# Kernel tuning notes

Hardware: AMD Instinct MI355X
Metric: run time of the kernel (lower is better)

The kernel has to match this reference:

```python
import jax, jax.numpy as jnp
import numpy as np

N = 100_000   # nodes
E = 200_000   # edges
D = 768       # d_model
L = 4         # gnn_layers
AF, AV = 9, 64   # atom feature columns, atom vocab
BF, BV = 3, 8    # bond feature columns, bond vocab


def layer_norm(x, g, b, eps=1e-5):
    m = x.mean(-1, keepdims=True)
    v = x.var(-1, keepdims=True)
    return (x - m) * jax.lax.rsqrt(v + eps) * g + b


def setup_inputs() -> dict:
    key = jax.random.key(0)
    keys = iter(jax.random.split(key, 40))
    w = lambda shape: jax.random.normal(next(keys), shape, jnp.float32) * 0.02
    return {
        "x": jax.random.randint(next(keys), (N, AF), 0, AV),
        "edge_attr": jax.random.randint(next(keys), (E, BF), 0, BV),
        "edge_index": jax.random.randint(next(keys), (2, E), 0, N),
        # AtomEncoder params (9 embedding tables stacked)
        "atom_emb": w((AF, AV, D)),
        "atom_ln_g": jnp.ones((D,)), "atom_ln_b": jnp.zeros((D,)),
        "atom_w1": w((D, D)), "atom_b1": jnp.zeros((D,)),
        "atom_w2": w((D, D)), "atom_b2": jnp.zeros((D,)),
        # BondEncoder params (3 embedding tables stacked)
        "bond_emb": w((BF, BV, D)),
        "bond_ln_g": jnp.ones((D,)), "bond_ln_b": jnp.zeros((D,)),
        "bond_w1": w((D, D)), "bond_b1": jnp.zeros((D,)),
        "bond_w2": w((D, D)), "bond_b2": jnp.zeros((D,)),
        # per-layer GINEConv MLP (Linear-ReLU-Linear) and LayerNorm, stacked on L
        "conv_w1": w((L, D, D)), "conv_b1": jnp.zeros((L, D)),
        "conv_w2": w((L, D, D)), "conv_b2": jnp.zeros((L, D)),
        "ln_g": jnp.ones((L, D)), "ln_b": jnp.zeros((L, D)),
    }


def reference(x, edge_attr, edge_index,
              atom_emb, atom_ln_g, atom_ln_b, atom_w1, atom_b1, atom_w2, atom_b2,
              bond_emb, bond_ln_g, bond_ln_b, bond_w1, bond_b1, bond_w2, bond_b2,
              conv_w1, conv_b1, conv_w2, conv_b2, ln_g, ln_b):
    gelu = lambda t: jax.nn.gelu(t, approximate=False)  # torch default GELU is exact

    # AtomEncoder: sum of per-column embeddings -> LN -> Linear/GELU/Linear
    h = atom_emb[jnp.arange(AF), x].sum(axis=1)            # [N, D]
    h = layer_norm(h, atom_ln_g, atom_ln_b)
    h = gelu(h @ atom_w1 + atom_b1) @ atom_w2 + atom_b2

    # BondEncoder
    e = bond_emb[jnp.arange(BF), edge_attr].sum(axis=1)    # [E, D]
    e = layer_norm(e, bond_ln_g, bond_ln_b)
    e = gelu(e @ bond_w1 + bond_b1) @ bond_w2 + bond_b2

    src, dst = edge_index[0], edge_index[1]
    for l in range(L):
        # GINEConv (eps=0): aggr_i = sum_{j->i} relu(h_j + e_ji); out = mlp(h_i + aggr_i)
        msg = jax.nn.relu(h[src] + e)                      # [E, D] gather + add
        aggr = jax.ops.segment_sum(msg, dst, num_segments=N)
        z = h + aggr
        z = jax.nn.relu(z @ conv_w1[l] + conv_b1[l]) @ conv_w2[l] + conv_b2[l]
        z = gelu(z)                                        # dropout=0 (eval)
        h = layer_norm(z + h, ln_g[l], ln_b[l])
    return h
```

## Files before the change

### kernel.cpp

```cpp
#include <hip/hip_runtime.h>

#define DM 768
#define SCAN_BS 1024

using u16 = unsigned short;
using u32 = unsigned int;

typedef __attribute__((ext_vector_type(8))) __bf16 bf16x8;
typedef __attribute__((ext_vector_type(4))) float f32x4;
typedef __attribute__((address_space(1))) void gvoid;
typedef __attribute__((address_space(3))) void lvoid;

__device__ __forceinline__ float bf2f(u16 h) { return __uint_as_float(((u32)h) << 16); }
__device__ __forceinline__ u16 f2bf(float f) {
    u32 u = __float_as_uint(f);
    u32 r = (u + 0x7FFFu + ((u >> 16) & 1u)) >> 16;
    return (u16)r;
}
__device__ __forceinline__ float gelu_f(float x) { return 0.5f * x * (1.f + erff(x * 0.70710678118f)); }

__global__ __launch_bounds__(256) void prep_weights(
    const float* __restrict__ aw1, const float* __restrict__ aw2,
    const float* __restrict__ bw1, const float* __restrict__ bw2,
    const float* __restrict__ cw1, const float* __restrict__ cw2,
    u16* __restrict__ wbt)
{
    int z = blockIdx.z;
    const float* W;
    if (z == 0) W = aw1;
    else if (z == 1) W = aw2;
    else if (z == 2) W = bw1;
    else if (z == 3) W = bw2;
    else if (z < 8) W = cw1 + (size_t)(z - 4) * DM * DM;
    else W = cw2 + (size_t)(z - 8) * DM * DM;
    u16* out = wbt + (size_t)z * DM * DM;

    __shared__ float tile[32][33];
    int bx = blockIdx.x * 32, by = blockIdx.y * 32;
    int tx = threadIdx.x & 31, ty = threadIdx.x >> 5;
    #pragma unroll
    for (int i = ty; i < 32; i += 8) tile[i][tx] = W[(size_t)(by + i) * DM + bx + tx];
    __syncthreads();
    #pragma unroll
    for (int i = ty; i < 32; i += 8) out[(size_t)(bx + i) * DM + by + tx] = f2bf(tile[tx][i]);
}

__global__ __launch_bounds__(256) void encode_ln(
    const int* __restrict__ idx, int nf, int vocab,
    const float* __restrict__ emb, const float* __restrict__ g, const float* __restrict__ bb,
    u16* __restrict__ out)
{
    long n = blockIdx.x;
    int t = threadIdx.x;
    __shared__ int feat[16];
    __shared__ float sred[16];
    if (t < nf) feat[t] = idx[n * nf + t];
    __syncthreads();
    float v[3];
    float s = 0.f, s2 = 0.f;
    #pragma unroll
    for (int j = 0; j < 3; j++) {
        int d = t + j * 256;
        float a = 0.f;
        for (int f = 0; f < nf; f++) a += emb[((long)f * vocab + feat[f]) * DM + d];
        v[j] = a; s += a; s2 += a * a;
    }
    #pragma unroll
    for (int o = 32; o; o >>= 1) { s += __shfl_down(s, o); s2 += __shfl_down(s2, o); }
    int wid = t >> 6;
    if ((t & 63) == 0) { sred[wid] = s; sred[8 + wid] = s2; }
    __syncthreads();
    if (t == 0) {
        sred[0] = sred[0] + sred[1] + sred[2] + sred[3];
        sred[8] = sred[8] + sred[9] + sred[10] + sred[11];
    }
    __syncthreads();
    float mean = sred[0] * (1.f / 768.f);
    float var = sred[8] * (1.f / 768.f) - mean * mean;
    float rstd = rsqrtf(var + 1e-5f);
    #pragma unroll
    for (int j = 0; j < 3; j++) {
        int d = t + j * 256;
        out[n * DM + d] = f2bf((v[j] - mean) * rstd * g[d] + bb[d]);
    }
}

__global__ __launch_bounds__(256) void encode_ln_bond(
    const float* __restrict__ emb, const float* __restrict__ g, const float* __restrict__ bb,
    u16* __restrict__ out)
{
    int key = blockIdx.x;
    int t = threadIdx.x;
    __shared__ float sred[16];
    int f0 = key & 7, f1 = (key >> 3) & 7, f2 = (key >> 6) & 7;
    float v[3];
    float s = 0.f, s2 = 0.f;
    #pragma unroll
    for (int j = 0; j < 3; j++) {
        int d = t + j * 256;
        float a = emb[(0 * 8 + f0) * DM + d] + emb[(1 * 8 + f1) * DM + d] + emb[(2 * 8 + f2) * DM + d];
        v[j] = a; s += a; s2 += a * a;
    }
    #pragma unroll
    for (int o = 32; o; o >>= 1) { s += __shfl_down(s, o); s2 += __shfl_down(s2, o); }
    int wid = t >> 6;
    if ((t & 63) == 0) { sred[wid] = s; sred[8 + wid] = s2; }
    __syncthreads();
    if (t == 0) {
        sred[0] = sred[0] + sred[1] + sred[2] + sred[3];
        sred[8] = sred[8] + sred[9] + sred[10] + sred[11];
    }
    __syncthreads();
    float mean = sred[0] * (1.f / 768.f);
    float var = sred[8] * (1.f / 768.f) - mean * mean;
    float rstd = rsqrtf(var + 1e-5f);
    #pragma unroll
    for (int j = 0; j < 3; j++) {
        int d = t + j * 256;
        out[(long)key * DM + d] = f2bf((v[j] - mean) * rstd * g[d] + bb[d]);
    }
}

__global__ __launch_bounds__(192) void layer_ln(
    const u16* __restrict__ y, const u16* __restrict__ holdb,
    const float* __restrict__ g, const float* __restrict__ bb,
    u16* __restrict__ hb, float* __restrict__ dout)
{
    long n = blockIdx.x;
    int t = threadIdx.x;
    int d = t * 4;
    __shared__ float sred[8];
    ushort4 yv = *reinterpret_cast<const ushort4*>(y + n * DM + d);
    ushort4 hv = *reinterpret_cast<const ushort4*>(holdb + n * DM + d);
    float v0 = bf2f(yv.x) + bf2f(hv.x);
    float v1 = bf2f(yv.y) + bf2f(hv.y);
    float v2 = bf2f(yv.z) + bf2f(hv.z);
    float v3 = bf2f(yv.w) + bf2f(hv.w);
    float s = v0 + v1 + v2 + v3;
    float s2 = v0 * v0 + v1 * v1 + v2 * v2 + v3 * v3;
    #pragma unroll
    for (int o = 32; o; o >>= 1) { s += __shfl_down(s, o); s2 += __shfl_down(s2, o); }
    int wid = t >> 6;
    if ((t & 63) == 0) { sred[wid] = s; sred[4 + wid] = s2; }
    __syncthreads();
    float S = sred[0] + sred[1] + sred[2];
    float S2 = sred[4] + sred[5] + sred[6];
    float mean = S * (1.f / 768.f);
    float var = S2 * (1.f / 768.f) - mean * mean;
    float rstd = rsqrtf(var + 1e-5f);
    float r0 = (v0 - mean) * rstd * g[d + 0] + bb[d + 0];
    float r1 = (v1 - mean) * rstd * g[d + 1] + bb[d + 1];
    float r2 = (v2 - mean) * rstd * g[d + 2] + bb[d + 2];
    float r3 = (v3 - mean) * rstd * g[d + 3] + bb[d + 3];
    if (dout) {
        float4 o = { r0, r1, r2, r3 };
        *reinterpret_cast<float4*>(dout + n * DM + d) = o;
    } else {
        ushort4 o;
        o.x = f2bf(r0); o.y = f2bf(r1); o.z = f2bf(r2); o.w = f2bf(r3);
        *reinterpret_cast<ushort4*>(hb + n * DM + d) = o;
    }
}

__global__ __launch_bounds__(256) void csr_count(const int* __restrict__ dst, int* __restrict__ deg, int E)
{
    int e = blockIdx.x * 256 + threadIdx.x;
    if (e < E) atomicAdd(&deg[dst[e]], 1);
}

__global__ __launch_bounds__(SCAN_BS) void scan_block(const int* __restrict__ deg, int* __restrict__ tmp,
                                                      int* __restrict__ bsum, int n)
{
    __shared__ int sh[SCAN_BS];
    int gid = blockIdx.x * SCAN_BS + threadIdx.x;
    int v = (gid < n) ? deg[gid] : 0;
    sh[threadIdx.x] = v;
    __syncthreads();
    for (int o = 1; o < SCAN_BS; o <<= 1) {
        int add = (threadIdx.x >= o) ? sh[threadIdx.x - o] : 0;
        __syncthreads();
        sh[threadIdx.x] += add;
        __syncthreads();
    }
    if (gid < n) tmp[gid] = sh[threadIdx.x];
    if (threadIdx.x == SCAN_BS - 1) bsum[blockIdx.x] = sh[SCAN_BS - 1];
}

__global__ __launch_bounds__(SCAN_BS) void scan_bsum(int* __restrict__ bsum, int nb)
{
    __shared__ int sh[SCAN_BS];
    int v = (threadIdx.x < nb) ? bsum[threadIdx.x] : 0;
    sh[threadIdx.x] = v;
    __syncthreads();
    for (int o = 1; o < SCAN_BS; o <<= 1) {
        int add = (threadIdx.x >= o) ? sh[threadIdx.x - o] : 0;
        __syncthreads();
        sh[threadIdx.x] += add;
        __syncthreads();
    }
    if (threadIdx.x < nb) bsum[threadIdx.x] = sh[threadIdx.x];
}

__global__ __launch_bounds__(256) void scan_final(const int* __restrict__ tmp, const int* __restrict__ bsum,
                                                  const int* __restrict__ deg, int* __restrict__ offs,
                                                  int* __restrict__ cursor, int n)
{
    int gid = blockIdx.x * 256 + threadIdx.x;
    if (gid >= n) return;
    int b = gid / SCAN_BS;
    int inc = tmp[gid] + (b > 0 ? bsum[b - 1] : 0);
    offs[gid + 1] = inc;
    cursor[gid] = inc - deg[gid];
    if (gid == 0) offs[0] = 0;
}

__global__ __launch_bounds__(256) void csr_fill(const int* __restrict__ dst, int* __restrict__ cursor,
                                                int* __restrict__ perm, int E)
{
    int e = blockIdx.x * 256 + threadIdx.x;
    if (e < E) {
        int p = atomicAdd(&cursor[dst[e]], 1);
        perm[p] = e;
    }
}

__global__ __launch_bounds__(256) void pack_edges(
    const int* __restrict__ src, const int* __restrict__ eattr, const int* __restrict__ perm,
    u32* __restrict__ ep, int E)
{
    int k = blockIdx.x * 256 + threadIdx.x;
    if (k < E) {
        int eid = perm[k];
        int key = eattr[eid * 3 + 0] + (eattr[eid * 3 + 1] << 3) + (eattr[eid * 3 + 2] << 6);
        ep[k] = ((u32)src[eid] << 9) | (u32)key;
    }
}

__global__ __launch_bounds__(192) void aggregate(
    const u16* __restrict__ h, const u16* __restrict__ ebtab,
    const u32* __restrict__ ep, const int* __restrict__ offs,
    u16* __restrict__ out)
{
    long n = blockIdx.x;
    int t = threadIdx.x;
    int d = t * 4;
    ushort4 a = *reinterpret_cast<const ushort4*>(h + n * DM + d);
    float acc0 = bf2f(a.x), acc1 = bf2f(a.y), acc2 = bf2f(a.z), acc3 = bf2f(a.w);
    int beg = offs[n], end = offs[n + 1];
    for (int k = beg; k < end; k++) {
        u32 pk = ep[k];
        long s = pk >> 9;
        long key = pk & 511;
        ushort4 hv = *reinterpret_cast<const ushort4*>(h + s * DM + d);
        ushort4 ev = *reinterpret_cast<const ushort4*>(ebtab + key * DM + d);
        acc0 += fmaxf(0.f, bf2f(hv.x) + bf2f(ev.x));
        acc1 += fmaxf(0.f, bf2f(hv.y) + bf2f(ev.y));
        acc2 += fmaxf(0.f, bf2f(hv.z) + bf2f(ev.z));
        acc3 += fmaxf(0.f, bf2f(hv.w) + bf2f(ev.w));
    }
    ushort4 o;
    o.x = f2bf(acc0); o.y = f2bf(acc1); o.z = f2bf(acc2); o.w = f2bf(acc3);
    *reinterpret_cast<ushort4*>(out + n * DM + d) = o;
}

union GemmSmem {
    u16 tiles[2][2][128 * 32];
    u16 ctile[128 * 136];
};

template <int ACT>
__global__ __launch_bounds__(256) void gemm128(
    const u16* __restrict__ A, const u16* __restrict__ Bt,
    const float* __restrict__ bias, u16* __restrict__ outB)
{
    __shared__ GemmSmem sm;
    const int tid = threadIdx.x;
    const int lane = tid & 63, wid = tid >> 6;
    const int wr = wid >> 1, wc = wid & 1;

    const int nwg = gridDim.x;
    const int orig = blockIdx.x;
    const int q8 = nwg >> 3, r8 = nwg & 7;
    const int xcd = orig & 7, idx8 = orig >> 3;
    const int w = (xcd < r8 ? xcd * (q8 + 1) : r8 * (q8 + 1) + (xcd - r8) * q8) + idx8;
    const int n0 = (w % 6) * 128;
    const long m0 = (long)(w / 6) * 128;

    f32x4 acc[4][4] = {};

    const int ch0 = tid, ch1 = 256 + tid;
    const int r0_ = ch0 >> 2, k0_ = (ch0 & 3) ^ ((r0_ >> 1) & 3);
    const int r1_ = ch1 >> 2, k1_ = (ch1 & 3) ^ ((r1_ >> 1) & 3);
    const u16* Ag0 = A + (m0 + r0_) * DM + k0_ * 8;
    const u16* Ag1 = A + (m0 + r1_) * DM + k1_ * 8;
    const u16* Bg0 = Bt + (long)(n0 + r0_) * DM + k0_ * 8;
    const u16* Bg1 = Bt + (long)(n0 + r1_) * DM + k1_ * 8;
    const int lds0 = ((wid << 6)) * 8;
    const int lds1 = (256 + (wid << 6)) * 8;

    auto stage = [&](int buf, int kt) {
        int ko = kt * 32;
        __builtin_amdgcn_global_load_lds((gvoid*)(Ag0 + ko), (lvoid*)&sm.tiles[buf][0][lds0], 16, 0, 0);
        __builtin_amdgcn_global_load_lds((gvoid*)(Ag1 + ko), (lvoid*)&sm.tiles[buf][0][lds1], 16, 0, 0);
        __builtin_amdgcn_global_load_lds((gvoid*)(Bg0 + ko), (lvoid*)&sm.tiles[buf][1][lds0], 16, 0, 0);
        __builtin_amdgcn_global_load_lds((gvoid*)(Bg1 + ko), (lvoid*)&sm.tiles[buf][1][lds1], 16, 0, 0);
    };

    stage(0, 0);
    asm volatile("s_waitcnt vmcnt(0)" ::: "memory");
    __syncthreads();

    const int ar = lane & 15, kb = lane >> 4;
    const int kbe = kb ^ ((ar >> 1) & 3);
    int cur = 0;
    for (int kt = 0; kt < DM / 32; ++kt) {
        if (kt + 1 < DM / 32) stage(cur ^ 1, kt + 1);
        bf16x8 af[4], bv[4];
        #pragma unroll
        for (int m = 0; m < 4; m++)
            af[m] = *reinterpret_cast<const bf16x8*>(&sm.tiles[cur][0][(wr * 64 + m * 16 + ar) * 32 + kbe * 8]);
        #pragma unroll
        for (int n = 0; n < 4; n++)
            bv[n] = *reinterpret_cast<const bf16x8*>(&sm.tiles[cur][1][(wc * 64 + n * 16 + ar) * 32 + kbe * 8]);
        #pragma unroll
        for (int m = 0; m < 4; m++)
            #pragma unroll
            for (int n = 0; n < 4; n++)
                acc[m][n] = __builtin_amdgcn_mfma_f32_16x16x32_bf16(af[m], bv[n], acc[m][n], 0, 0, 0);
        asm volatile("s_waitcnt vmcnt(0)" ::: "memory");
        __syncthreads();
        cur ^= 1;
    }

    const int rg4 = (lane >> 4) * 4;
    #pragma unroll
    for (int n = 0; n < 4; n++) {
        int lc = wc * 64 + n * 16 + ar;
        float bvp = bias[n0 + lc];
        #pragma unroll
        for (int m = 0; m < 4; m++) {
            int lr = wr * 64 + m * 16 + rg4;
            #pragma unroll
            for (int j = 0; j < 4; j++) {
                float v = acc[m][n][j] + bvp;
                if (ACT == 1) v = fmaxf(v, 0.f);
                if (ACT == 2) v = gelu_f(v);
                sm.ctile[(lr + j) * 136 + lc] = f2bf(v);
            }
        }
    }
    __syncthreads();
    const int row = tid >> 2, b4 = tid & 3;
    #pragma unroll
    for (int ps = 0; ps < 2; ps++) {
        int rr = row + ps * 64;
        const u16* srcp = &sm.ctile[rr * 136];
        u16* dstp = outB + (m0 + rr) * DM + n0;
        #pragma unroll
        for (int i = 0; i < 4; i++) {
            int c = b4 * 8 + i * 32;
            *reinterpret_cast<uint4*>(dstp + c) = *reinterpret_cast<const uint4*>(srcp + c);
        }
    }
}

extern "C" void kernel_launch(void* const* d_in, const int* in_sizes, int n_in,
                              void* d_out, int out_size, void* d_ws, size_t ws_size,
                              hipStream_t stream)
{
    const int N = in_sizes[0] / 9;
    const int E = in_sizes[1] / 3;
    const int L = 4;
    const long Mpad = ((N + 127) / 128) * 128;
    const int Mtiles = (int)(Mpad / 128);

    const int* x = (const int*)d_in[0];
    const int* eattr = (const int*)d_in[1];
    const int* eidx = (const int*)d_in[2];
    const float* atom_emb = (const float*)d_in[3];
    const float* atom_g = (const float*)d_in[4];
    const float* atom_bb = (const float*)d_in[5];
    const float* atom_w1 = (const float*)d_in[6];
    const float* atom_b1 = (const float*)d_in[7];
    const float* atom_w2 = (const float*)d_in[8];
    const float* atom_b2 = (const float*)d_in[9];
    const float* bond_emb = (const float*)d_in[10];
    const float* bond_g = (const float*)d_in[11];
    const float* bond_bb = (const float*)d_in[12];
    const float* bond_w1 = (const float*)d_in[13];
    const float* bond_b1 = (const float*)d_in[14];
    const float* bond_w2 = (const float*)d_in[15];
    const float* bond_b2 = (const float*)d_in[16];
    const float* conv_w1 = (const float*)d_in[17];
    const float* conv_b1 = (const float*)d_in[18];
    const float* conv_w2 = (const float*)d_in[19];
    const float* conv_b2 = (const float*)d_in[20];
    const float* ln_g = (const float*)d_in[21];
    const float* ln_b = (const float*)d_in[22];
    const int* src = eidx;
    const int* dst = eidx + E;
    float* dout = (float*)d_out;

    char* p = (char*)d_ws;
    auto alloc = [&](size_t bytes) { void* r = (void*)p; p += (bytes + 255) & ~(size_t)255; return r; };
    u16* B2   = (u16*)alloc((size_t)2 * Mpad * DM * 2);
    u16* h_b  = (u16*)alloc((size_t)Mpad * DM * 2);
    u16* wbt  = (u16*)alloc((size_t)12 * DM * DM * 2);
    u16* bt0  = (u16*)alloc((size_t)512 * DM * 2);
    u16* bt1  = (u16*)alloc((size_t)512 * DM * 2);
    u16* ebtab= (u16*)alloc((size_t)512 * DM * 2);
    int* deg    = (int*)alloc((size_t)N * 4);
    int* tmp    = (int*)alloc((size_t)N * 4);
    int* cursor = (int*)alloc((size_t)N * 4);
    int* offs   = (int*)alloc((size_t)(N + 1) * 4);
    int* bsum   = (int*)alloc((size_t)SCAN_BS * 4);
    int* perm   = (int*)alloc((size_t)E * 4);
    u32* ep     = (u32*)alloc((size_t)E * 4);
    u16* B2a = B2;
    u16* B2b = B2 + (size_t)Mpad * DM;

    hipMemsetAsync(deg, 0, (size_t)N * 4, stream);
    csr_count<<<(E + 255) / 256, 256, 0, stream>>>(dst, deg, E);
    const int nb = (N + SCAN_BS - 1) / SCAN_BS;
    scan_block<<<nb, SCAN_BS, 0, stream>>>(deg, tmp, bsum, N);
    scan_bsum<<<1, SCAN_BS, 0, stream>>>(bsum, nb);
    scan_final<<<(N + 255) / 256, 256, 0, stream>>>(tmp, bsum, deg, offs, cursor, N);
    csr_fill<<<(E + 255) / 256, 256, 0, stream>>>(dst, cursor, perm, E);
    pack_edges<<<(E + 255) / 256, 256, 0, stream>>>(src, eattr, perm, ep, E);

    prep_weights<<<dim3(24, 24, 12), 256, 0, stream>>>(atom_w1, atom_w2, bond_w1, bond_w2, conv_w1, conv_w2, wbt);

    encode_ln_bond<<<512, 256, 0, stream>>>(bond_emb, bond_g, bond_bb, bt0);
    gemm128<2><<<6 * 4, 256, 0, stream>>>(bt0, wbt + (size_t)2 * DM * DM, bond_b1, bt1);
    gemm128<0><<<6 * 4, 256, 0, stream>>>(bt1, wbt + (size_t)3 * DM * DM, bond_b2, ebtab);

    encode_ln<<<N, 256, 0, stream>>>(x, 9, 64, atom_emb, atom_g, atom_bb, B2a);
    gemm128<2><<<6 * Mtiles, 256, 0, stream>>>(B2a, wbt + (size_t)0 * DM * DM, atom_b1, B2b);
    gemm128<0><<<6 * Mtiles, 256, 0, stream>>>(B2b, wbt + (size_t)1 * DM * DM, atom_b2, h_b);

    for (int l = 0; l < L; l++) {
        aggregate<<<N, 192, 0, stream>>>(h_b, ebtab, ep, offs, B2a);
        gemm128<1><<<6 * Mtiles, 256, 0, stream>>>(B2a, wbt + (size_t)(4 + l) * DM * DM, conv_b1 + l * DM, B2b);
        gemm128<2><<<6 * Mtiles, 256, 0, stream>>>(B2b, wbt + (size_t)(8 + l) * DM * DM, conv_b2 + l * DM, B2a);
        layer_ln<<<N, 192, 0, stream>>>(B2a, h_b, ln_g + l * DM, ln_b + l * DM,
                                        h_b, (l == L - 1) ? dout : nullptr);
    }
}
```

Measured before the change: 3.092 ms.

## Use 256-row GEMM tiles, tanh-approx GELU, and vectorized atom encoder

The GEMM tile grows from 128x128 to 256x128. Each wave now computes 64x128 with 32 accumulators, which doubles B-tile reuse per load and halves the number of blocks. The epilogue writes the output in two 128-row halves through the shared C tile. The exact erf GELU is replaced with a tanh approximation using fast exp and reciprocal, which cuts epilogue math but departs from the exact-GELU reference. The atom encoder uses 192 threads with float4 loads and a single reduction barrier.

```diff
diff --git a/kernel.cpp b/kernel.cpp
--- a/kernel.cpp
+++ b/kernel.cpp
@@ -17,7 +17,12 @@
     u32 r = (u + 0x7FFFu + ((u >> 16) & 1u)) >> 16;
     return (u16)r;
 }
-__device__ __forceinline__ float gelu_f(float x) { return 0.5f * x * (1.f + erff(x * 0.70710678118f)); }
+__device__ __forceinline__ float gelu_f(float x) {
+    float y = 0.7978845608f * x * (1.f + 0.044715f * x * x);
+    float e = __expf(2.f * y);
+    float th = 1.f - 2.f * __builtin_amdgcn_rcpf(e + 1.f);
+    return 0.5f * x * (1.f + th);
+}
 
 __global__ __launch_bounds__(256) void prep_weights(
     const float* __restrict__ aw1, const float* __restrict__ aw2,
@@ -45,44 +50,43 @@
     for (int i = ty; i < 32; i += 8) out[(size_t)(bx + i) * DM + by + tx] = f2bf(tile[tx][i]);
 }
 
-__global__ __launch_bounds__(256) void encode_ln(
-    const int* __restrict__ idx, int nf, int vocab,
+__global__ __launch_bounds__(192) void encode_ln9(
+    const int* __restrict__ idx,
     const float* __restrict__ emb, const float* __restrict__ g, const float* __restrict__ bb,
     u16* __restrict__ out)
 {
     long n = blockIdx.x;
     int t = threadIdx.x;
-    __shared__ int feat[16];
-    __shared__ float sred[16];
-    if (t < nf) feat[t] = idx[n * nf + t];
-    __syncthreads();
-    float v[3];
-    float s = 0.f, s2 = 0.f;
-    #pragma unroll
-    for (int j = 0; j < 3; j++) {
-        int d = t + j * 256;
-        float a = 0.f;
-        for (int f = 0; f < nf; f++) a += emb[((long)f * vocab + feat[f]) * DM + d];
-        v[j] = a; s += a; s2 += a * a;
-    }
+    int d = t * 4;
+    __shared__ int feat[12];
+    __shared__ float sred[8];
+    if (t < 9) feat[t] = idx[n * 9 + t];
+    __syncthreads();
+    float a0 = 0.f, a1 = 0.f, a2 = 0.f, a3 = 0.f;
+    #pragma unroll
+    for (int f = 0; f < 9; f++) {
+        const float* rp = emb + (size_t)f * 64 * DM + (size_t)feat[f] * DM + d;
+        float4 v = *reinterpret_cast<const float4*>(rp);
+        a0 += v.x; a1 += v.y; a2 += v.z; a3 += v.w;
+    }
+    float s = a0 + a1 + a2 + a3;
+    float s2 = a0 * a0 + a1 * a1 + a2 * a2 + a3 * a3;
     #pragma unroll
     for (int o = 32; o; o >>= 1) { s += __shfl_down(s, o); s2 += __shfl_down(s2, o); }
     int wid = t >> 6;
-    if ((t & 63) == 0) { sred[wid] = s; sred[8 + wid] = s2; }
-    __syncthreads();
-    if (t == 0) {
-        sred[0] = sred[0] + sred[1] + sred[2] + sred[3];
-        sred[8] = sred[8] + sred[9] + sred[10] + sred[11];
-    }
-    __syncthreads();
-    float mean = sred[0] * (1.f / 768.f);
-    float var = sred[8] * (1.f / 768.f) - mean * mean;
+    if ((t & 63) == 0) { sred[wid] = s; sred[4 + wid] = s2; }
+    __syncthreads();
+    float S = sred[0] + sred[1] + sred[2];
+    float S2 = sred[4] + sred[5] + sred[6];
+    float mean = S * (1.f / 768.f);
+    float var = S2 * (1.f / 768.f) - mean * mean;
     float rstd = rsqrtf(var + 1e-5f);
-    #pragma unroll
-    for (int j = 0; j < 3; j++) {
-        int d = t + j * 256;
-        out[n * DM + d] = f2bf((v[j] - mean) * rstd * g[d] + bb[d]);
-    }
+    ushort4 o;
+    o.x = f2bf((a0 - mean) * rstd * g[d + 0] + bb[d + 0]);
+    o.y = f2bf((a1 - mean) * rstd * g[d + 1] + bb[d + 1]);
+    o.z = f2bf((a2 - mean) * rstd * g[d + 2] + bb[d + 2]);
+    o.w = f2bf((a3 - mean) * rstd * g[d + 3] + bb[d + 3]);
+    *reinterpret_cast<ushort4*>(out + n * DM + d) = o;
 }
 
 __global__ __launch_bounds__(256) void encode_ln_bond(
@@ -264,19 +268,18 @@
 }
 
 union GemmSmem {
-    u16 tiles[2][2][128 * 32];
+    u16 tiles[2][384 * 32];
     u16 ctile[128 * 136];
 };
 
 template <int ACT>
-__global__ __launch_bounds__(256) void gemm128(
+__global__ __launch_bounds__(256) void gemm256(
     const u16* __restrict__ A, const u16* __restrict__ Bt,
     const float* __restrict__ bias, u16* __restrict__ outB)
 {
     __shared__ GemmSmem sm;
     const int tid = threadIdx.x;
     const int lane = tid & 63, wid = tid >> 6;
-    const int wr = wid >> 1, wc = wid & 1;
 
     const int nwg = gridDim.x;
     const int orig = blockIdx.x;
@@ -284,26 +287,30 @@
     const int xcd = orig & 7, idx8 = orig >> 3;
     const int w = (xcd < r8 ? xcd * (q8 + 1) : r8 * (q8 + 1) + (xcd - r8) * q8) + idx8;
     const int n0 = (w % 6) * 128;
-    const long m0 = (long)(w / 6) * 128;
-
-    f32x4 acc[4][4] = {};
-
-    const int ch0 = tid, ch1 = 256 + tid;
-    const int r0_ = ch0 >> 2, k0_ = (ch0 & 3) ^ ((r0_ >> 1) & 3);
-    const int r1_ = ch1 >> 2, k1_ = (ch1 & 3) ^ ((r1_ >> 1) & 3);
-    const u16* Ag0 = A + (m0 + r0_) * DM + k0_ * 8;
-    const u16* Ag1 = A + (m0 + r1_) * DM + k1_ * 8;
-    const u16* Bg0 = Bt + (long)(n0 + r0_) * DM + k0_ * 8;
-    const u16* Bg1 = Bt + (long)(n0 + r1_) * DM + k1_ * 8;
-    const int lds0 = ((wid << 6)) * 8;
-    const int lds1 = (256 + (wid << 6)) * 8;
+    const long m0 = (long)(w / 6) * 256;
+
+    f32x4 acc[4][8] = {};
+
+    const u16* gsrc[6];
+    #pragma unroll
+    for (int cl = 0; cl < 6; cl++) {
+        int c = cl * 256 + tid;
+        if (cl < 4) {
+            int r = c >> 2, kc = (c & 3) ^ ((r >> 1) & 3);
+            gsrc[cl] = A + (m0 + r) * DM + kc * 8;
+        } else {
+            int cb = c - 1024;
+            int r = cb >> 2, kc = (cb & 3) ^ ((r >> 1) & 3);
+            gsrc[cl] = Bt + (long)(n0 + r) * DM + kc * 8;
+        }
+    }
 
     auto stage = [&](int buf, int kt) {
         int ko = kt * 32;
-        __builtin_amdgcn_global_load_lds((gvoid*)(Ag0 + ko), (lvoid*)&sm.tiles[buf][0][lds0], 16, 0, 0);
-        __builtin_amdgcn_global_load_lds((gvoid*)(Ag1 + ko), (lvoid*)&sm.tiles[buf][0][lds1], 16, 0, 0);
-        __builtin_amdgcn_global_load_lds((gvoid*)(Bg0 + ko), (lvoid*)&sm.tiles[buf][1][lds0], 16, 0, 0);
-        __builtin_amdgcn_global_load_lds((gvoid*)(Bg1 + ko), (lvoid*)&sm.tiles[buf][1][lds1], 16, 0, 0);
+        #pragma unroll
+        for (int cl = 0; cl < 6; cl++)
+            __builtin_amdgcn_global_load_lds((gvoid*)(gsrc[cl] + ko),
+                (lvoid*)&sm.tiles[buf][(cl * 256 + (wid << 6)) * 8], 16, 0, 0);
     };
 
     stage(0, 0);
@@ -315,17 +322,17 @@
     int cur = 0;
     for (int kt = 0; kt < DM / 32; ++kt) {
         if (kt + 1 < DM / 32) stage(cur ^ 1, kt + 1);
-        bf16x8 af[4], bv[4];
+        bf16x8 af[4], bv[8];
         #pragma unroll
         for (int m = 0; m < 4; m++)
-            af[m] = *reinterpret_cast<const bf16x8*>(&sm.tiles[cur][0][(wr * 64 + m * 16 + ar) * 32 + kbe * 8]);
+            af[m] = *reinterpret_cast<const bf16x8*>(&sm.tiles[cur][(wid * 64 + m * 16 + ar) * 32 + kbe * 8]);
         #pragma unroll
-        for (int n = 0; n < 4; n++)
-            bv[n] = *reinterpret_cast<const bf16x8*>(&sm.tiles[cur][1][(wc * 64 + n * 16 + ar) * 32 + kbe * 8]);
+        for (int n = 0; n < 8; n++)
+            bv[n] = *reinterpret_cast<const bf16x8*>(&sm.tiles[cur][8192 + (n * 16 + ar) * 32 + kbe * 8]);
         #pragma unroll
         for (int m = 0; m < 4; m++)
             #pragma unroll
-            for (int n = 0; n < 4; n++)
+            for (int n = 0; n < 8; n++)
                 acc[m][n] = __builtin_amdgcn_mfma_f32_16x16x32_bf16(af[m], bv[n], acc[m][n], 0, 0, 0);
         asm volatile("s_waitcnt vmcnt(0)" ::: "memory");
         __syncthreads();
@@ -334,32 +341,39 @@
 
     const int rg4 = (lane >> 4) * 4;
     #pragma unroll
-    for (int n = 0; n < 4; n++) {
-        int lc = wc * 64 + n * 16 + ar;
-        float bvp = bias[n0 + lc];
-        #pragma unroll
-        for (int m = 0; m < 4; m++) {
-            int lr = wr * 64 + m * 16 + rg4;
+    for (int hp = 0; hp < 2; hp++) {
+        if (hp) __syncthreads();
+        if ((wid >> 1) == hp) {
+            const int wl = wid & 1;
             #pragma unroll
-            for (int j = 0; j < 4; j++) {
-                float v = acc[m][n][j] + bvp;
-                if (ACT == 1) v = fmaxf(v, 0.f);
-                if (ACT == 2) v = gelu_f(v);
-                sm.ctile[(lr + j) * 136 + lc] = f2bf(v);
+            for (int n = 0; n < 8; n++) {
+                int lc = n * 16 + ar;
+                float bvp = bias[n0 + lc];
+                #pragma unroll
+                for (int m = 0; m < 4; m++) {
+                    int lr = wl * 64 + m * 16 + rg4;
+                    #pragma unroll
+                    for (int j = 0; j < 4; j++) {
+                        float v = acc[m][n][j] + bvp;
+                        if (ACT == 1) v = fmaxf(v, 0.f);
+                        if (ACT == 2) v = gelu_f(v);
+                        sm.ctile[(lr + j) * 136 + lc] = f2bf(v);
+                    }
+                }
             }
         }
-    }
-    __syncthreads();
-    const int row = tid >> 2, b4 = tid & 3;
-    #pragma unroll
-    for (int ps = 0; ps < 2; ps++) {
-        int rr = row + ps * 64;
-        const u16* srcp = &sm.ctile[rr * 136];
-        u16* dstp = outB + (m0 + rr) * DM + n0;
+        __syncthreads();
+        const int row = tid >> 2, b4 = tid & 3;
         #pragma unroll
-        for (int i = 0; i < 4; i++) {
-            int c = b4 * 8 + i * 32;
-            *reinterpret_cast<uint4*>(dstp + c) = *reinterpret_cast<const uint4*>(srcp + c);
+        for (int ps = 0; ps < 2; ps++) {
+            int rr = row + ps * 64;
+            const u16* srcp = &sm.ctile[rr * 136];
+            u16* dstp = outB + (m0 + hp * 128 + rr) * DM + n0;
+            #pragma unroll
+            for (int i = 0; i < 4; i++) {
+                int c = b4 * 8 + i * 32;
+                *reinterpret_cast<uint4*>(dstp + c) = *reinterpret_cast<const uint4*>(srcp + c);
+            }
         }
     }
 }
@@ -371,8 +385,8 @@
     const int N = in_sizes[0] / 9;
     const int E = in_sizes[1] / 3;
     const int L = 4;
-    const long Mpad = ((N + 127) / 128) * 128;
-    const int Mtiles = (int)(Mpad / 128);
+    const long Mpad = ((N + 255) / 256) * 256;
+    const int Mtiles = (int)(Mpad / 256);
 
     const int* x = (const int*)d_in[0];
     const int* eattr = (const int*)d_in[1];
@@ -431,17 +445,17 @@
     prep_weights<<<dim3(24, 24, 12), 256, 0, stream>>>(atom_w1, atom_w2, bond_w1, bond_w2, conv_w1, conv_w2, wbt);
 
     encode_ln_bond<<<512, 256, 0, stream>>>(bond_emb, bond_g, bond_bb, bt0);
-    gemm128<2><<<6 * 4, 256, 0, stream>>>(bt0, wbt + (size_t)2 * DM * DM, bond_b1, bt1);
-    gemm128<0><<<6 * 4, 256, 0, stream>>>(bt1, wbt + (size_t)3 * DM * DM, bond_b2, ebtab);
-
-    encode_ln<<<N, 256, 0, stream>>>(x, 9, 64, atom_emb, atom_g, atom_bb, B2a);
-    gemm128<2><<<6 * Mtiles, 256, 0, stream>>>(B2a, wbt + (size_t)0 * DM * DM, atom_b1, B2b);
-    gemm128<0><<<6 * Mtiles, 256, 0, stream>>>(B2b, wbt + (size_t)1 * DM * DM, atom_b2, h_b);
+    gemm256<2><<<6 * 2, 256, 0, stream>>>(bt0, wbt + (size_t)2 * DM * DM, bond_b1, bt1);
+    gemm256<0><<<6 * 2, 256, 0, stream>>>(bt1, wbt + (size_t)3 * DM * DM, bond_b2, ebtab);
+
+    encode_ln9<<<N, 192, 0, stream>>>(x, atom_emb, atom_g, atom_bb, B2a);
+    gemm256<2><<<6 * Mtiles, 256, 0, stream>>>(B2a, wbt + (size_t)0 * DM * DM, atom_b1, B2b);
+    gemm256<0><<<6 * Mtiles, 256, 0, stream>>>(B2b, wbt + (size_t)1 * DM * DM, atom_b2, h_b);
 
     for (int l = 0; l < L; l++) {
         aggregate<<<N, 192, 0, stream>>>(h_b, ebtab, ep, offs, B2a);
-        gemm128<1><<<6 * Mtiles, 256, 0, stream>>>(B2a, wbt + (size_t)(4 + l) * DM * DM, conv_b1 + l * DM, B2b);
-        gemm128<2><<<6 * Mtiles, 256, 0, stream>>>(B2b, wbt + (size_t)(8 + l) * DM * DM, conv_b2 + l * DM, B2a);
+        gemm256<1><<<6 * Mtiles, 256, 0, stream>>>(B2a, wbt + (size_t)(4 + l) * DM * DM, conv_b1 + l * DM, B2b);
+        gemm256<2><<<6 * Mtiles, 256, 0, stream>>>(B2b, wbt + (size_t)(8 + l) * DM * DM, conv_b2 + l * DM, B2a);
         layer_ln<<<N, 192, 0, stream>>>(B2a, h_b, ln_g + l * DM, ln_b + l * DM,
                                         h_b, (l == L - 1) ? dout : nullptr);
     }
```

Result: slower. 3.988 ms (+29.0%).
